# Performance work log

Measured on AMD Instinct MI355X. Metric: run time of the kernel, lower is better.

The kernel has to match this reference:

```python
import jax, jax.numpy as jnp
import numpy as np

B, V, C, G, D, H, W, N = 1, 4, 32, 8, 8, 240, 320, 9
EPS = 1e-5  # BatchNorm3d default eps


def grid_sample(img, grid, align_corners, zeros_pad):
    # img [B,C,Hs,Ws], grid [B,Hg,Wg,2] normalized coords; mirrors torch F.grid_sample bilinear
    Bi, Ci, Hs, Ws = img.shape
    gx, gy = grid[..., 0], grid[..., 1]
    if align_corners:
        ix = (gx + 1.0) * 0.5 * (Ws - 1)
        iy = (gy + 1.0) * 0.5 * (Hs - 1)
    else:
        ix = ((gx + 1.0) * Ws - 1.0) * 0.5
        iy = ((gy + 1.0) * Hs - 1.0) * 0.5
    x0 = jnp.floor(ix)
    y0 = jnp.floor(iy)
    wx1 = ix - x0
    wy1 = iy - y0

    def corner(xi, yi, wgt):
        xc = jnp.clip(xi, 0, Ws - 1).astype(jnp.int32)
        yc = jnp.clip(yi, 0, Hs - 1).astype(jnp.int32)
        v = jax.vmap(lambda im, yy, xx: im[:, yy, xx])(img, yc, xc)  # [B,C,Hg,Wg]
        if zeros_pad:
            valid = ((xi >= 0) & (xi <= Ws - 1) & (yi >= 0) & (yi <= Hs - 1)).astype(img.dtype)
            wgt = wgt * valid
        return v * wgt[:, None]

    return (corner(x0, y0, (1 - wx1) * (1 - wy1)) + corner(x0 + 1, y0, wx1 * (1 - wy1))
            + corner(x0, y0 + 1, (1 - wx1) * wy1) + corner(x0 + 1, y0 + 1, wx1 * wy1))


def differentiable_warping(src_fea, src_proj, ref_proj, depth):
    # src_fea [B,Cf,H,W], projs [B,4,4], depth [B,D,H,W] -> [B,Cf,D,H,W]
    Bi, Cf, Hs, Ws = src_fea.shape
    Dd = depth.shape[1]
    proj = src_proj @ jnp.linalg.inv(ref_proj)
    rot, trans = proj[:, :3, :3], proj[:, :3, 3:4]
    yy, xx = jnp.meshgrid(jnp.arange(Hs, dtype=jnp.float32), jnp.arange(Ws, dtype=jnp.float32), indexing='ij')
    xyz = jnp.stack([xx.ravel(), yy.ravel(), jnp.ones(Hs * Ws, jnp.float32)], axis=0)  # [3,HW]
    rot_xyz = jnp.einsum('bij,jk->bik', rot, xyz)  # [B,3,HW]
    pxyz = rot_xyz[:, :, None, :] * depth.reshape(Bi, 1, Dd, Hs * Ws) + trans[:, :, :, None]  # [B,3,D,HW]
    neg = pxyz[:, 2] <= 1e-3
    px = jnp.where(neg, float(Ws), pxyz[:, 0])
    py = jnp.where(neg, float(Hs), pxyz[:, 1])
    pz = jnp.where(neg, 1.0, pxyz[:, 2])
    gx = (px / pz) / ((Ws - 1) / 2.0) - 1.0
    gy = (py / pz) / ((Hs - 1) / 2.0) - 1.0
    grid = jnp.stack([gx, gy], axis=-1).reshape(Bi, Dd * Hs, Ws, 2)
    grid = jax.lax.stop_gradient(grid)  # torch builds the warp grid under no_grad
    warped = grid_sample(src_fea, grid, align_corners=True, zeros_pad=True)  # [B,Cf,D*H,W]
    return warped.reshape(Bi, Cf, Dd, Hs, Ws)


def conv_bn_relu(x, w, bn):
    # 1x1x1 Conv3d (no bias) + BatchNorm3d (inference) + ReLU; x [B,Ci,D,H,W]
    y = jnp.einsum('oi,bidhw->bodhw', w, x)
    g, b, m, v = bn
    s = g / jnp.sqrt(v + EPS)
    return jax.nn.relu(y * s[:, None, None, None] + (b - m * s)[:, None, None, None])


def conv1(x, w, b):
    return jnp.einsum('oi,bidhw->bodhw', w, x) + b[:, None, None, None]


def pixel_wise_net(sim, w0, bn0, w1, bn1, w2, b2):
    y = conv_bn_relu(sim, w0, bn0)
    y = conv_bn_relu(y, w1, bn1)
    y = jax.nn.sigmoid(conv1(y, w2, b2))[:, 0]  # [B,D,H,W]
    return jnp.max(y, axis=1, keepdims=True)  # [B,1,H,W]


def _forward(ref_feature, src_features, ref_proj, src_projs, depth_sample, grid, weight,
             pw_w0, pw_bn0, pw_w1, pw_bn1, pw_w2, pw_b2,
             sn_w0, sn_bn0, sn_w1, sn_bn1, sn_w2, sn_b2):
    Bi, Cf, Hs, Ws = ref_feature.shape
    Gq = pw_w0.shape[1]
    Dd = depth_sample.shape[1]
    ref_g = ref_feature.reshape(Bi, Gq, Cf // Gq, 1, Hs, Ws)
    sim_sum = jnp.zeros((Bi, Gq, Dd, Hs, Ws), jnp.float32)
    w_sum = jnp.zeros((Bi, 1, 1, Hs, Ws), jnp.float32)
    vws = []
    for v in range(src_features.shape[0]):  # small fixed view count
        warped = differentiable_warping(src_features[v], src_projs[v], ref_proj, depth_sample)
        warped = warped.reshape(Bi, Gq, Cf // Gq, Dd, Hs, Ws)
        sim = jnp.mean(warped * ref_g, axis=2)  # [B,G,D,H,W] group correlation
        vw = pixel_wise_net(sim, pw_w0, pw_bn0, pw_w1, pw_bn1, pw_w2, pw_b2)  # [B,1,H,W]
        vws.append(vw)
        sim_sum = sim_sum + sim * vw[:, :, None]
        w_sum = w_sum + vw[:, :, None]
    x = sim_sum / w_sum
    # SimilarityNet: conv stack -> neighbor grid_sample -> adaptive weighted sum
    y = conv_bn_relu(x, sn_w0, sn_bn0)
    y = conv_bn_relu(y, sn_w1, sn_bn1)
    y = conv1(y, sn_w2, sn_b2)[:, 0]  # [B,D,H,W]
    s = grid_sample(y, grid, align_corners=False, zeros_pad=False)  # border pad, [B,D,N*H,W]
    Nn = grid.shape[1] // Hs
    s = s.reshape(Bi, Dd, Nn, Hs, Ws)
    score_vol = jnp.sum(s * weight, axis=2)  # [B,D,H,W]
    score = jax.nn.softmax(score_vol, axis=1)  # exp(log_softmax) == softmax
    depth = jnp.sum(depth_sample * score, axis=1)  # [B,H,W] (is_inverse=False)
    view_weights = jax.lax.stop_gradient(jnp.concatenate(vws, axis=1))  # [B,V,H,W]
    return depth, score, view_weights


def setup_inputs():
    key = jax.random.key(0)
    ks = jax.random.split(key, 20)
    ref_feature = jax.random.normal(ks[0], (B, C, H, W), jnp.float32)
    src_features = jax.random.normal(ks[1], (V, B, C, H, W), jnp.float32)
    f = 500.0
    K = np.array([[f, 0, W / 2.0, 0], [0, f, H / 2.0, 0], [0, 0, 1, 0], [0, 0, 0, 1]], np.float32)
    ref_proj = jnp.asarray(np.tile(K[None], (B, 1, 1)))
    sp = []
    for tx, ty in [(20.0, 0.0), (-20.0, 0.0), (0.0, 10.0), (0.0, -10.0)]:
        E = np.eye(4, dtype=np.float32)
        E[0, 3], E[1, 3] = tx, ty
        sp.append(np.tile((K @ E)[None], (B, 1, 1)))
    src_projs = jnp.asarray(np.stack(sp))
    depth_sample = jnp.sort(425.0 + 510.0 * jax.random.uniform(ks[2], (B, D, H, W), jnp.float32), axis=1)
    # evaluation neighbor grid: per-pixel +-3px learned-style offsets, align_corners=False normalization
    dx = jax.random.uniform(ks[3], (B, N, H, W), minval=-3.0, maxval=3.0)
    dy = jax.random.uniform(ks[4], (B, N, H, W), minval=-3.0, maxval=3.0)
    xs = jnp.arange(W, dtype=jnp.float32)[None, None, None, :]
    ys = jnp.arange(H, dtype=jnp.float32)[None, None, :, None]
    gx = (2.0 * (xs + dx) + 1.0) / W - 1.0
    gy = (2.0 * (ys + dy) + 1.0) / H - 1.0
    grid = jnp.stack([gx, gy], -1).reshape(B, N * H, W, 2)
    weight = jax.random.uniform(ks[5], (B, D, N, H, W), jnp.float32)  # feature*depth weight in (0,1)

    def bn(k, c):
        k1, k2, k3, k4 = jax.random.split(k, 4)
        return jnp.stack([1.0 + 0.1 * jax.random.normal(k1, (c,)), 0.1 * jax.random.normal(k2, (c,)),
                          0.01 * jax.random.normal(k3, (c,)), 1.0 + 0.1 * jax.random.uniform(k4, (c,))])

    return dict(ref_feature=ref_feature, src_features=src_features, ref_proj=ref_proj,
                src_projs=src_projs, depth_sample=depth_sample, grid=grid, weight=weight,
                pw_w0=0.1 * jax.random.normal(ks[6], (16, G)), pw_bn0=bn(ks[7], 16),
                pw_w1=0.1 * jax.random.normal(ks[8], (8, 16)), pw_bn1=bn(ks[9], 8),
                pw_w2=0.1 * jax.random.normal(ks[10], (1, 8)), pw_b2=jnp.zeros((1,), jnp.float32),
                sn_w0=0.1 * jax.random.normal(ks[11], (16, G)), sn_bn0=bn(ks[12], 16),
                sn_w1=0.1 * jax.random.normal(ks[13], (8, 16)), sn_bn1=bn(ks[14], 8),
                sn_w2=0.1 * jax.random.normal(ks[15], (1, 8)), sn_b2=jnp.zeros((1,), jnp.float32))


def reference(ref_feature, src_features, ref_proj, src_projs, depth_sample, grid, weight,
              pw_w0, pw_bn0, pw_w1, pw_bn1, pw_w2, pw_b2,
              sn_w0, sn_bn0, sn_w1, sn_bn1, sn_w2, sn_b2):
    return _forward(ref_feature, src_features, ref_proj, src_projs, depth_sample, grid, weight,
                    pw_w0, pw_bn0, pw_w1, pw_bn1, pw_w2, pw_b2,
                    sn_w0, sn_bn0, sn_w1, sn_bn1, sn_w2, sn_b2)
```

## Files before the change

### kernel.cpp

```cpp
#include <hip/hip_runtime.h>
#include <hip/hip_fp16.h>
#include <cstdint>
#include <cstddef>

#define HH 240
#define WW 320
#define HWPIX 76800
#define NVIEW 4
#define NCH 32
#define NGRP 8
#define NDEP 8
#define NNEI 9
#define QPLANE (HWPIX * 8)

#define OFF_TAB 64
#define OFF_Y    4096
#define OFF_SRCT 618496
#define OFF_DEPT 6762496

typedef _Float16 h2 __attribute__((ext_vector_type(2)));
typedef __fp16  h8v __attribute__((ext_vector_type(8)));
typedef float f32x16 __attribute__((ext_vector_type(16)));

__device__ __forceinline__ float fdot2_(h2 a, h2 b, float c) {
#if __has_builtin(__builtin_amdgcn_fdot2)
  return __builtin_amdgcn_fdot2(a, b, c, false);
#else
  return c + (float)a.x * (float)b.x + (float)a.y * (float)b.y;
#endif
}
__device__ __forceinline__ h2 pk_(float a, float b) {
#if __has_builtin(__builtin_amdgcn_cvt_pkrtz)
  return __builtin_bit_cast(h2, __builtin_amdgcn_cvt_pkrtz(a, b));
#else
  h2 r; r.x = (_Float16)a; r.y = (_Float16)b; return r;
#endif
}
__device__ __forceinline__ float pkf_(float a, float b) {
  return __builtin_bit_cast(float, pk_(a, b));
}

__device__ __forceinline__ f32x16 mfma_(h8v a, h8v b, f32x16 c) {
  return __builtin_amdgcn_mfma_f32_32x32x16_f16(a, b, c, 0, 0, 0);
}

__device__ __forceinline__ float mlp_mfma(float4 x4, h8v w0f, h8v w1f,
                                          float4 b1s, float4 w2s, float b2v,
                                          bool lo) {
  f32x16 Z = {};
  float4 xsw;
  xsw.x = __shfl_xor(x4.x, 32, 64);
  xsw.y = __shfl_xor(x4.y, 32, 64);
  xsw.z = __shfl_xor(x4.z, 32, 64);
  xsw.w = __shfl_xor(x4.w, 32, 64);
  float4 cst;
  cst.x = __builtin_bit_cast(float, 0x00003C00u);
  cst.y = 0.0f; cst.z = 0.0f; cst.w = 0.0f;
  float4 blo, bhi;
  blo.x = lo ? x4.x : cst.x;  blo.y = lo ? x4.y : cst.y;
  blo.z = lo ? x4.z : cst.z;  blo.w = lo ? x4.w : cst.w;
  bhi.x = lo ? xsw.x : cst.x; bhi.y = lo ? xsw.y : cst.y;
  bhi.z = lo ? xsw.z : cst.z; bhi.w = lo ? xsw.w : cst.w;

  float yv0 = 0.0f, yv1 = 0.0f;
#pragma unroll
  for (int bb = 0; bb < 2; ++bb) {
    float4 bin = bb ? bhi : blo;
    f32x16 acc = mfma_(w0f, __builtin_bit_cast(h8v, bin), Z);
    float dw0 = pkf_(fmaxf(acc[0], 0.f), fmaxf(acc[1], 0.f));
    float dw1 = pkf_(fmaxf(acc[2], 0.f), fmaxf(acc[3], 0.f));
    float dw2 = pkf_(fmaxf(acc[4], 0.f), fmaxf(acc[5], 0.f));
    float dw3 = pkf_(fmaxf(acc[6], 0.f), fmaxf(acc[7], 0.f));
    float s0 = __shfl_xor(dw0, 32, 64);
    float s1 = __shfl_xor(dw1, 32, 64);
    float s2 = __shfl_xor(dw2, 32, 64);
    float s3 = __shfl_xor(dw3, 32, 64);
    float4 bf;
    bf.x = lo ? dw0 : s2;
    bf.y = lo ? dw1 : s3;
    bf.z = lo ? s0 : dw2;
    bf.w = lo ? s1 : dw3;
    f32x16 a2 = mfma_(w1f, __builtin_bit_cast(h8v, bf), Z);
    float p = fmaxf(a2[0] + b1s.x, 0.f) * w2s.x;
    p = fmaf(fmaxf(a2[1] + b1s.y, 0.f), w2s.y, p);
    p = fmaf(fmaxf(a2[2] + b1s.z, 0.f), w2s.z, p);
    p = fmaf(fmaxf(a2[3] + b1s.w, 0.f), w2s.w, p);
    p += __shfl_xor(p, 32, 64);
    if (bb) yv1 = p + b2v; else yv0 = p + b2v;
  }
  return lo ? yv0 : yv1;
}

__global__ __launch_bounds__(256) void k_prep(
    const float* __restrict__ src, const float* __restrict__ ref,
    const float* __restrict__ depthS,
    __half* __restrict__ dst, float* __restrict__ dep_t,
    const float* __restrict__ refP, const float* __restrict__ srcP,
    const float* __restrict__ pw0, const float* __restrict__ pbn0,
    const float* __restrict__ pw1, const float* __restrict__ pbn1,
    const float* __restrict__ pw2, const float* __restrict__ pb2,
    const float* __restrict__ sw0, const float* __restrict__ sbn0,
    const float* __restrict__ sw1, const float* __restrict__ sbn1,
    const float* __restrict__ sw2, const float* __restrict__ sb2,
    float* __restrict__ ws, int nTransBlocks) {
  if ((int)blockIdx.x == nTransBlocks) {
    int tid = threadIdx.x;
    if (tid < 128) {
      int net = tid >> 6;
      int l = tid & 63;
      int n = l & 31;
      int hi = l >> 5;
      const float* W0 = net ? sw0 : pw0;  const float* B0 = net ? sbn0 : pbn0;
      const float* W1 = net ? sw1 : pw1;  const float* B1 = net ? sbn1 : pbn1;
      const float* W2 = net ? sw2 : pw2;
      float* base = ws + OFF_TAB + net * 1024;
      float4 r;
      if (hi == 0 && n < 16) {
        float s = B0[n] / sqrtf(B0[48 + n] + 1e-5f) * 0.25f;
        r.x = pkf_(W0[n * 8 + 0] * s, W0[n * 8 + 1] * s);
        r.y = pkf_(W0[n * 8 + 2] * s, W0[n * 8 + 3] * s);
        r.z = pkf_(W0[n * 8 + 4] * s, W0[n * 8 + 5] * s);
        r.w = pkf_(W0[n * 8 + 6] * s, W0[n * 8 + 7] * s);
      } else if (hi == 1 && n < 16) {
        float s = B0[n] / sqrtf(B0[48 + n] + 1e-5f);
        float b0f = B0[16 + n] - B0[32 + n] * s;
        r.x = pkf_(b0f, 0.f); r.y = 0.f; r.z = 0.f; r.w = 0.f;
      } else { r.x = r.y = r.z = r.w = 0.f; }
      ((float4*)(base))[l] = r;
      float4 q;
      if (n < 8) {
        float s = B1[n] / sqrtf(B1[24 + n] + 1e-5f);
        int o = n * 16 + 8 * hi;
        q.x = pkf_(W1[o + 0] * s, W1[o + 1] * s);
        q.y = pkf_(W1[o + 2] * s, W1[o + 3] * s);
        q.z = pkf_(W1[o + 4] * s, W1[o + 5] * s);
        q.w = pkf_(W1[o + 6] * s, W1[o + 7] * s);
      } else { q.x = q.y = q.z = q.w = 0.f; }
      ((float4*)(base + 256))[l] = q;
      float4 b;
      {
        float bb[4];
        for (int rr = 0; rr < 4; ++rr) {
          int o = rr + 4 * hi;
          float s = B1[o] / sqrtf(B1[24 + o] + 1e-5f);
          bb[rr] = B1[8 + o] - B1[16 + o] * s;
        }
        b.x = bb[0]; b.y = bb[1]; b.z = bb[2]; b.w = bb[3];
      }
      ((float4*)(base + 512))[l] = b;
      float4 w2v;
      w2v.x = W2[0 + 4 * hi]; w2v.y = W2[1 + 4 * hi];
      w2v.z = W2[2 + 4 * hi]; w2v.w = W2[3 + 4 * hi];
      ((float4*)(base + 768))[l] = w2v;
    } else if (tid == 128) {
      ws[62] = pb2[0];
      ws[63] = sb2[0];
    } else if (tid == 129) {
      float a[4][8];
      for (int i = 0; i < 4; ++i)
        for (int j = 0; j < 4; ++j) { a[i][j] = refP[i * 4 + j]; a[i][4 + j] = (i == j) ? 1.0f : 0.0f; }
      for (int c = 0; c < 4; ++c) {
        int piv = c; float best = fabsf(a[c][c]);
        for (int r2 = c + 1; r2 < 4; ++r2) { float t = fabsf(a[r2][c]); if (t > best) { best = t; piv = r2; } }
        if (piv != c) for (int j = 0; j < 8; ++j) { float t = a[c][j]; a[c][j] = a[piv][j]; a[piv][j] = t; }
        float inv = 1.0f / a[c][c];
        for (int j = 0; j < 8; ++j) a[c][j] *= inv;
        for (int r2 = 0; r2 < 4; ++r2) if (r2 != c) {
          float f = a[r2][c];
          for (int j = 0; j < 8; ++j) a[r2][j] -= f * a[c][j];
        }
      }
      for (int v = 0; v < NVIEW; ++v) {
        const float* S = srcP + v * 16;
        for (int i = 0; i < 3; ++i)
          for (int j = 0; j < 4; ++j) {
            float p = S[i*4+0]*a[0][4+j] + S[i*4+1]*a[1][4+j] + S[i*4+2]*a[2][4+j] + S[i*4+3]*a[3][4+j];
            if (j < 3) ws[v * 12 + i * 3 + j] = p;
            else       ws[v * 12 + 9 + i] = p;
          }
      }
    }
    return;
  }
  int t = blockIdx.x * 256 + threadIdx.x;
  const int base = 20 * HWPIX;
  if (t >= base) {
    int pix = t - base;
    float4 a, b;
    a.x = depthS[0 * HWPIX + pix]; a.y = depthS[1 * HWPIX + pix];
    a.z = depthS[2 * HWPIX + pix]; a.w = depthS[3 * HWPIX + pix];
    b.x = depthS[4 * HWPIX + pix]; b.y = depthS[5 * HWPIX + pix];
    b.z = depthS[6 * HWPIX + pix]; b.w = depthS[7 * HWPIX + pix];
    float4* o = reinterpret_cast<float4*>(dep_t + (size_t)pix * NDEP);
    o[0] = a; o[1] = b;
    return;
  }
  int vq = t / HWPIX;
  int pix = t - vq * HWPIX;
  int v = vq >> 2;
  int q = vq & 3;
  const float* s = (v < NVIEW) ? (src + ((size_t)(v * NCH + q * 8)) * HWPIX + pix)
                               : (ref + ((size_t)(q * 8)) * HWPIX + pix);
  union { h2 h[4]; float4 f; } u;
  u.h[0] = pk_(s[0],         s[HWPIX]);
  u.h[1] = pk_(s[2 * HWPIX], s[3 * HWPIX]);
  u.h[2] = pk_(s[4 * HWPIX], s[5 * HWPIX]);
  u.h[3] = pk_(s[6 * HWPIX], s[7 * HWPIX]);
  reinterpret_cast<float4*>(dst + (size_t)vq * QPLANE)[pix] = u.f;
}

__device__ __forceinline__ void tapq(const __half* __restrict__ p, float wtf,
                                     h2* __restrict__ wp, bool first) {
  _Float16 wh = (_Float16)wtf;
  h2 wt2 = h2{wh, wh};
  union { float4 f; h2 h[4]; } u;
  u.f = *reinterpret_cast<const float4*>(p);
#pragma unroll
  for (int c = 0; c < 4; ++c) {
    if (first) wp[c] = u.h[c] * wt2;
    else       wp[c] += u.h[c] * wt2;
  }
}

__global__ __launch_bounds__(512) void k_main(
    const __half* __restrict__ srcT, const float* __restrict__ depthS,
    const float* __restrict__ wsc,
    float* __restrict__ ybuf, float* __restrict__ outVW) {
  __shared__ float sred[NDEP * 64];
  int tid = threadIdx.x;
  int lane = tid & 63;
  int d = tid >> 6;
  bool lo = lane < 32;
  int pix = blockIdx.x * 64 + lane;
  int h = pix / WW;
  int w = pix - h * WW;
  float fx = (float)w, fy = (float)h;

  h8v w0f_pw = ((const h8v*)(wsc + OFF_TAB))[lane];
  h8v w1f_pw = ((const h8v*)(wsc + OFF_TAB + 256))[lane];
  float4 b1s_pw = ((const float4*)(wsc + OFF_TAB + 512))[lane];
  float4 w2s_pw = ((const float4*)(wsc + OFF_TAB + 768))[lane];
  float b2_pw = wsc[62];

  h2 rc[16];
  {
    const __half* refb = srcT + (size_t)16 * QPLANE;
#pragma unroll
    for (int q = 0; q < 4; ++q) {
      union { float4 f; h2 hh[4]; } u;
      u.f = *reinterpret_cast<const float4*>(refb + (size_t)q * QPLANE + (size_t)pix * 8);
      rc[4*q] = u.hh[0]; rc[4*q+1] = u.hh[1]; rc[4*q+2] = u.hh[2]; rc[4*q+3] = u.hh[3];
    }
  }
  float dep = depthS[d * HWPIX + pix];

  float ssum[NGRP];
#pragma unroll
  for (int g = 0; g < NGRP; ++g) ssum[g] = 0.0f;
  float wsum = 0.0f;

#pragma unroll 1
  for (int v = 0; v < NVIEW; ++v) {
    const float* pr = wsc + v * 12;
    float rx = fmaf(pr[0], fx, fmaf(pr[1], fy, pr[2]));
    float ry = fmaf(pr[3], fx, fmaf(pr[4], fy, pr[5]));
    float rz = fmaf(pr[6], fx, fmaf(pr[7], fy, pr[8]));
    float pz_ = fmaf(rz, dep, pr[11]);
    bool neg = (pz_ <= 0.001f);
    float px_ = neg ? (float)WW : fmaf(rx, dep, pr[9]);
    float py_ = neg ? (float)HH : fmaf(ry, dep, pr[10]);
    float rpz = neg ? 1.0f : __fdividef(1.0f, pz_);
    float ix = px_ * rpz;
    float iy = py_ * rpz;
    float x0f = floorf(ix), y0f = floorf(iy);
    float wx1 = ix - x0f, wy1 = iy - y0f;
    float wx0 = 1.0f - wx1, wy0 = 1.0f - wy1;
    float x1f = x0f + 1.0f, y1f = y0f + 1.0f;
    float vx0 = (x0f >= 0.0f && x0f <= (float)(WW - 1)) ? 1.0f : 0.0f;
    float vx1 = (x1f >= 0.0f && x1f <= (float)(WW - 1)) ? 1.0f : 0.0f;
    float vy0 = (y0f >= 0.0f && y0f <= (float)(HH - 1)) ? 1.0f : 0.0f;
    float vy1 = (y1f >= 0.0f && y1f <= (float)(HH - 1)) ? 1.0f : 0.0f;
    int xa = (int)fminf(fmaxf(x0f, 0.0f), (float)(WW - 1));
    int xb = (int)fminf(fmaxf(x1f, 0.0f), (float)(WW - 1));
    int ya = (int)fminf(fmaxf(y0f, 0.0f), (float)(HH - 1));
    int yb = (int)fminf(fmaxf(y1f, 0.0f), (float)(HH - 1));
    float w00 = wx0 * wy0 * vx0 * vy0;
    float w01 = wx1 * wy0 * vx1 * vy0;
    float w10 = wx0 * wy1 * vx0 * vy1;
    float w11 = wx1 * wy1 * vx1 * vy1;

    int t00 = ya * WW + xa, t01 = ya * WW + xb;
    int t10 = yb * WW + xa, t11 = yb * WW + xb;

    float simf[NGRP];
    {
      const __half* vb = srcT + (size_t)(v * 4) * QPLANE;
      h2 wp[16];
#pragma unroll
      for (int q = 0; q < 4; ++q) {
        const __half* pb = vb + (size_t)q * QPLANE;
        tapq(pb + (size_t)t00 * 8, w00, wp + 4 * q, true);
        tapq(pb + (size_t)t01 * 8, w01, wp + 4 * q, false);
        tapq(pb + (size_t)t10 * 8, w10, wp + 4 * q, false);
        tapq(pb + (size_t)t11 * 8, w11, wp + 4 * q, false);
      }
#pragma unroll
      for (int g = 0; g < NGRP; ++g)
        simf[g] = fdot2_(wp[2*g+1], rc[2*g+1], fdot2_(wp[2*g], rc[2*g], 0.0f));
    }

    float4 xp;
    xp.x = pkf_(simf[0], simf[1]);
    xp.y = pkf_(simf[2], simf[3]);
    xp.z = pkf_(simf[4], simf[5]);
    xp.w = pkf_(simf[6], simf[7]);
    float sc = mlp_mfma(xp, w0f_pw, w1f_pw, b1s_pw, w2s_pw, b2_pw, lo);

    sred[(d << 6) | lane] = sc;
    __syncthreads();
    float m = sred[lane];
#pragma unroll
    for (int j = 1; j < NDEP; ++j) m = fmaxf(m, sred[(j << 6) | lane]);
    __syncthreads();
    float vw = __fdividef(1.0f, 1.0f + __expf(-m));

#pragma unroll
    for (int g = 0; g < NGRP; ++g) ssum[g] = fmaf(simf[g], vw, ssum[g]);
    wsum += vw;
    if (d == 0) outVW[v * HWPIX + pix] = vw;
  }

  float rw = __fdividef(1.0f, wsum);
  float4 xg;
  xg.x = pkf_(ssum[0] * rw, ssum[1] * rw);
  xg.y = pkf_(ssum[2] * rw, ssum[3] * rw);
  xg.z = pkf_(ssum[4] * rw, ssum[5] * rw);
  xg.w = pkf_(ssum[6] * rw, ssum[7] * rw);
  h8v w0f_sn = ((const h8v*)(wsc + OFF_TAB + 1024))[lane];
  h8v w1f_sn = ((const h8v*)(wsc + OFF_TAB + 1024 + 256))[lane];
  float4 b1s_sn = ((const float4*)(wsc + OFF_TAB + 1024 + 512))[lane];
  float4 w2s_sn = ((const float4*)(wsc + OFF_TAB + 1024 + 768))[lane];
  float b2_sn = wsc[63];
  float yv = mlp_mfma(xg, w0f_sn, w1f_sn, b1s_sn, w2s_sn, b2_sn, lo);
  ybuf[pix * NDEP + d] = yv;
}

__global__ __launch_bounds__(256) void k_score(
    const float* __restrict__ grid, const float* __restrict__ weight,
    const float* __restrict__ dep_t, const float* __restrict__ ybuf,
    float* __restrict__ out) {
  int pix = blockIdx.x * 256 + threadIdx.x;
  int h = pix / WW;
  int w = pix - h * WW;
  float sv[NDEP];
#pragma unroll
  for (int d = 0; d < NDEP; ++d) sv[d] = 0.0f;

#pragma unroll 1
  for (int n = 0; n < NNEI; ++n) {
    int gi = ((n * HH + h) * WW + w) * 2;
    float gx = grid[gi], gy = grid[gi + 1];
    float ix = ((gx + 1.0f) * (float)WW - 1.0f) * 0.5f;
    float iy = ((gy + 1.0f) * (float)HH - 1.0f) * 0.5f;
    float x0f = floorf(ix), y0f = floorf(iy);
    float wx1 = ix - x0f, wy1 = iy - y0f;
    float wx0 = 1.0f - wx1, wy0 = 1.0f - wy1;
    int xa = (int)fminf(fmaxf(x0f, 0.0f), (float)(WW - 1));
    int xb = (int)fminf(fmaxf(x0f + 1.0f, 0.0f), (float)(WW - 1));
    int ya = (int)fminf(fmaxf(y0f, 0.0f), (float)(HH - 1));
    int yb2 = (int)fminf(fmaxf(y0f + 1.0f, 0.0f), (float)(HH - 1));
    const float4* p00 = reinterpret_cast<const float4*>(ybuf + (size_t)(ya * WW + xa) * NDEP);
    const float4* p01 = reinterpret_cast<const float4*>(ybuf + (size_t)(ya * WW + xb) * NDEP);
    const float4* p10 = reinterpret_cast<const float4*>(ybuf + (size_t)(yb2 * WW + xa) * NDEP);
    const float4* p11 = reinterpret_cast<const float4*>(ybuf + (size_t)(yb2 * WW + xb) * NDEP);
    float4 a00 = p00[0], b00 = p00[1];
    float4 a01 = p01[0], b01 = p01[1];
    float4 a10 = p10[0], b10 = p10[1];
    float4 a11 = p11[0], b11 = p11[1];
    const float* v00 = (const float*)&a00;
    const float* v01 = (const float*)&a01;
    const float* v10 = (const float*)&a10;
    const float* v11 = (const float*)&a11;
    const float* u00 = (const float*)&b00;
    const float* u01 = (const float*)&b01;
    const float* u10 = (const float*)&b10;
    const float* u11 = (const float*)&b11;
#pragma unroll
    for (int d = 0; d < NDEP; ++d) {
      float c00 = (d < 4) ? v00[d] : u00[d - 4];
      float c01 = (d < 4) ? v01[d] : u01[d - 4];
      float c10 = (d < 4) ? v10[d] : u10[d - 4];
      float c11 = (d < 4) ? v11[d] : u11[d - 4];
      float s = wy0 * fmaf(wx0, c00, wx1 * c01) + wy1 * fmaf(wx0, c10, wx1 * c11);
      float wn = weight[((size_t)(d * NNEI + n) * HH + h) * WW + w];
      sv[d] = fmaf(s, wn, sv[d]);
    }
  }
  float m = sv[0];
#pragma unroll
  for (int d = 1; d < NDEP; ++d) m = fmaxf(m, sv[d]);
  float e[NDEP], s8 = 0.0f;
#pragma unroll
  for (int d = 0; d < NDEP; ++d) { e[d] = __expf(sv[d] - m); s8 += e[d]; }
  float r = __fdividef(1.0f, s8);
  const float4* dp4 = reinterpret_cast<const float4*>(dep_t + (size_t)pix * NDEP);
  float4 da = dp4[0], db = dp4[1];
  float dpv[NDEP] = {da.x, da.y, da.z, da.w, db.x, db.y, db.z, db.w};
  float dp = 0.0f;
#pragma unroll
  for (int d = 0; d < NDEP; ++d) {
    float sc = e[d] * r;
    out[HWPIX + d * HWPIX + pix] = sc;
    dp = fmaf(dpv[d], sc, dp);
  }
  out[pix] = dp;
}

extern "C" void kernel_launch(void* const* d_in, const int* in_sizes, int n_in,
                              void* d_out, int out_size, void* d_ws, size_t ws_size,
                              hipStream_t stream) {
  const float* ref    = (const float*)d_in[0];
  const float* src    = (const float*)d_in[1];
  const float* refP   = (const float*)d_in[2];
  const float* srcP   = (const float*)d_in[3];
  const float* depthS = (const float*)d_in[4];
  const float* grid   = (const float*)d_in[5];
  const float* weight = (const float*)d_in[6];
  float* out = (float*)d_out;
  float* ws  = (float*)d_ws;
  __half* srcT = (__half*)(ws + OFF_SRCT);
  float* dep_t = ws + OFF_DEPT;

  int transThreads = 20 * HWPIX + HWPIX;
  int nTransBlocks = transThreads / 256;

  k_prep<<<nTransBlocks + 1, 256, 0, stream>>>(
      src, ref, depthS, srcT, dep_t, refP, srcP,
      (const float*)d_in[7],  (const float*)d_in[8],
      (const float*)d_in[9],  (const float*)d_in[10],
      (const float*)d_in[11], (const float*)d_in[12],
      (const float*)d_in[13], (const float*)d_in[14],
      (const float*)d_in[15], (const float*)d_in[16],
      (const float*)d_in[17], (const float*)d_in[18],
      ws, nTransBlocks);
  k_main<<<HWPIX / 64, 512, 0, stream>>>(srcT, depthS, ws, ws + OFF_Y, out + 9 * HWPIX);
  k_score<<<HWPIX / 256, 256, 0, stream>>>(grid, weight, dep_t, ws + OFF_Y, out);
}
```

Before: 84.08 us.

## Batch per-view MLP and reductions to one barrier, swizzle blocks, drop depth transpose

The main kernel now runs all four views' sampling and pixel-wise MLP before a single shared-memory exchange, replacing two barriers per view. The per-view packed similarities are kept in registers for the later weighted sum, and shared memory grows fourfold. Block indices are swizzled so consecutive blocks map to distant pixel rows, likely to spread cache traffic. The depth transpose in the prep kernel is removed, and the score kernel reads depth planes directly with coalesced loads. The main trade-off is higher register pressure in the main kernel.

```diff
diff --git a/kernel.cpp b/kernel.cpp
--- a/kernel.cpp
+++ b/kernel.cpp
@@ -16,7 +16,6 @@
 #define OFF_TAB 64
 #define OFF_Y    4096
 #define OFF_SRCT 618496
-#define OFF_DEPT 6762496
 
 typedef _Float16 h2 __attribute__((ext_vector_type(2)));
 typedef __fp16  h8v __attribute__((ext_vector_type(8)));
@@ -93,8 +92,7 @@
 
 __global__ __launch_bounds__(256) void k_prep(
     const float* __restrict__ src, const float* __restrict__ ref,
-    const float* __restrict__ depthS,
-    __half* __restrict__ dst, float* __restrict__ dep_t,
+    __half* __restrict__ dst,
     const float* __restrict__ refP, const float* __restrict__ srcP,
     const float* __restrict__ pw0, const float* __restrict__ pbn0,
     const float* __restrict__ pw1, const float* __restrict__ pbn1,
@@ -183,18 +181,6 @@
     return;
   }
   int t = blockIdx.x * 256 + threadIdx.x;
-  const int base = 20 * HWPIX;
-  if (t >= base) {
-    int pix = t - base;
-    float4 a, b;
-    a.x = depthS[0 * HWPIX + pix]; a.y = depthS[1 * HWPIX + pix];
-    a.z = depthS[2 * HWPIX + pix]; a.w = depthS[3 * HWPIX + pix];
-    b.x = depthS[4 * HWPIX + pix]; b.y = depthS[5 * HWPIX + pix];
-    b.z = depthS[6 * HWPIX + pix]; b.w = depthS[7 * HWPIX + pix];
-    float4* o = reinterpret_cast<float4*>(dep_t + (size_t)pix * NDEP);
-    o[0] = a; o[1] = b;
-    return;
-  }
   int vq = t / HWPIX;
   int pix = t - vq * HWPIX;
   int v = vq >> 2;
@@ -226,12 +212,14 @@
     const __half* __restrict__ srcT, const float* __restrict__ depthS,
     const float* __restrict__ wsc,
     float* __restrict__ ybuf, float* __restrict__ outVW) {
-  __shared__ float sred[NDEP * 64];
+  __shared__ float sred[NVIEW * NDEP * 64];
   int tid = threadIdx.x;
   int lane = tid & 63;
   int d = tid >> 6;
   bool lo = lane < 32;
-  int pix = blockIdx.x * 64 + lane;
+  int bid = (int)blockIdx.x;
+  int swz = (bid & 7) * 150 + (bid >> 3);
+  int pix = swz * 64 + lane;
   int h = pix / WW;
   int w = pix - h * WW;
   float fx = (float)w, fy = (float)h;
@@ -254,12 +242,9 @@
   }
   float dep = depthS[d * HWPIX + pix];
 
-  float ssum[NGRP];
-#pragma unroll
-  for (int g = 0; g < NGRP; ++g) ssum[g] = 0.0f;
-  float wsum = 0.0f;
-
-#pragma unroll 1
+  float4 xps[NVIEW];
+  float scv[NVIEW];
+#pragma unroll
   for (int v = 0; v < NVIEW; ++v) {
     const float* pr = wsc + v * 12;
     float rx = fmaf(pr[0], fx, fmaf(pr[1], fy, pr[2]));
@@ -314,18 +299,36 @@
     xp.y = pkf_(simf[2], simf[3]);
     xp.z = pkf_(simf[4], simf[5]);
     xp.w = pkf_(simf[6], simf[7]);
-    float sc = mlp_mfma(xp, w0f_pw, w1f_pw, b1s_pw, w2s_pw, b2_pw, lo);
-
-    sred[(d << 6) | lane] = sc;
-    __syncthreads();
-    float m = sred[lane];
-#pragma unroll
-    for (int j = 1; j < NDEP; ++j) m = fmaxf(m, sred[(j << 6) | lane]);
-    __syncthreads();
+    xps[v] = xp;
+    scv[v] = mlp_mfma(xp, w0f_pw, w1f_pw, b1s_pw, w2s_pw, b2_pw, lo);
+  }
+
+#pragma unroll
+  for (int v = 0; v < NVIEW; ++v) sred[(v << 9) | (d << 6) | lane] = scv[v];
+  __syncthreads();
+
+  float ssum[NGRP];
+#pragma unroll
+  for (int g = 0; g < NGRP; ++g) ssum[g] = 0.0f;
+  float wsum = 0.0f;
+#pragma unroll
+  for (int v = 0; v < NVIEW; ++v) {
+    float m = sred[(v << 9) | lane];
+#pragma unroll
+    for (int j = 1; j < NDEP; ++j) m = fmaxf(m, sred[(v << 9) | (j << 6) | lane]);
     float vw = __fdividef(1.0f, 1.0f + __expf(-m));
-
-#pragma unroll
-    for (int g = 0; g < NGRP; ++g) ssum[g] = fmaf(simf[g], vw, ssum[g]);
+    h2 p0 = __builtin_bit_cast(h2, xps[v].x);
+    h2 p1 = __builtin_bit_cast(h2, xps[v].y);
+    h2 p2 = __builtin_bit_cast(h2, xps[v].z);
+    h2 p3 = __builtin_bit_cast(h2, xps[v].w);
+    ssum[0] = fmaf((float)p0.x, vw, ssum[0]);
+    ssum[1] = fmaf((float)p0.y, vw, ssum[1]);
+    ssum[2] = fmaf((float)p1.x, vw, ssum[2]);
+    ssum[3] = fmaf((float)p1.y, vw, ssum[3]);
+    ssum[4] = fmaf((float)p2.x, vw, ssum[4]);
+    ssum[5] = fmaf((float)p2.y, vw, ssum[5]);
+    ssum[6] = fmaf((float)p3.x, vw, ssum[6]);
+    ssum[7] = fmaf((float)p3.y, vw, ssum[7]);
     wsum += vw;
     if (d == 0) outVW[v * HWPIX + pix] = vw;
   }
@@ -347,7 +350,7 @@
 
 __global__ __launch_bounds__(256) void k_score(
     const float* __restrict__ grid, const float* __restrict__ weight,
-    const float* __restrict__ dep_t, const float* __restrict__ ybuf,
+    const float* __restrict__ depthS, const float* __restrict__ ybuf,
     float* __restrict__ out) {
   int pix = blockIdx.x * 256 + threadIdx.x;
   int h = pix / WW;
@@ -403,15 +406,12 @@
 #pragma unroll
   for (int d = 0; d < NDEP; ++d) { e[d] = __expf(sv[d] - m); s8 += e[d]; }
   float r = __fdividef(1.0f, s8);
-  const float4* dp4 = reinterpret_cast<const float4*>(dep_t + (size_t)pix * NDEP);
-  float4 da = dp4[0], db = dp4[1];
-  float dpv[NDEP] = {da.x, da.y, da.z, da.w, db.x, db.y, db.z, db.w};
   float dp = 0.0f;
 #pragma unroll
   for (int d = 0; d < NDEP; ++d) {
     float sc = e[d] * r;
     out[HWPIX + d * HWPIX + pix] = sc;
-    dp = fmaf(dpv[d], sc, dp);
+    dp = fmaf(depthS[d * HWPIX + pix], sc, dp);
   }
   out[pix] = dp;
 }
@@ -429,13 +429,12 @@
   float* out = (float*)d_out;
   float* ws  = (float*)d_ws;
   __half* srcT = (__half*)(ws + OFF_SRCT);
-  float* dep_t = ws + OFF_DEPT;
-
-  int transThreads = 20 * HWPIX + HWPIX;
+
+  int transThreads = 20 * HWPIX;
   int nTransBlocks = transThreads / 256;
 
   k_prep<<<nTransBlocks + 1, 256, 0, stream>>>(
-      src, ref, depthS, srcT, dep_t, refP, srcP,
+      src, ref, srcT, refP, srcP,
       (const float*)d_in[7],  (const float*)d_in[8],
       (const float*)d_in[9],  (const float*)d_in[10],
       (const float*)d_in[11], (const float*)d_in[12],
@@ -444,5 +443,5 @@
       (const float*)d_in[17], (const float*)d_in[18],
       ws, nTransBlocks);
   k_main<<<HWPIX / 64, 512, 0, stream>>>(srcT, depthS, ws, ws + OFF_Y, out + 9 * HWPIX);
-  k_score<<<HWPIX / 256, 256, 0, stream>>>(grid, weight, dep_t, ws + OFF_Y, out);
-}
+  k_score<<<HWPIX / 256, 256, 0, stream>>>(grid, weight, depthS, ws + OFF_Y, out);
+}
```

Result: no change. 83.18 us (-1.1%).
